# Kernel optimization log

Hardware: AMD Instinct MI355X
Metric: run time of the kernel (lower is better)

Reference implementation:

```python
import jax, jax.numpy as jnp
import numpy as np

DECAY = 0.99
EPS = 1e-05
THRESHOLD = 2.0
CODEBOOK_SIZE = 2048
DIM = 256


def setup_inputs() -> dict:
    key = jax.random.key(0)
    k1, k2, k3 = jax.random.split(key, 3)
    x = jax.random.normal(k1, (32, 1500, DIM), dtype=jnp.float32)
    # kaiming_uniform_ with a=0: bound = sqrt(6 / fan_in)
    bound = float(np.sqrt(6.0 / DIM))
    embed = jax.random.uniform(k2, (CODEBOOK_SIZE, DIM), dtype=jnp.float32,
                               minval=-bound, maxval=bound)
    # warm EMA state: positive cluster sizes, consistent embed_avg
    cluster_size = jax.random.uniform(k3, (CODEBOOK_SIZE,), dtype=jnp.float32,
                                      minval=0.0, maxval=200.0)
    embed_avg = embed * cluster_size[:, None]
    return {"x": x, "embed": embed, "cluster_size": cluster_size,
            "embed_avg": embed_avg}


def reference(x, embed, cluster_size, embed_avg):
    shape = x.shape
    K = embed.shape[0]
    xf = x.reshape(-1, shape[-1])                       # [N, D]

    # quantize: negative squared Euclidean distance, argmax == argmin dist
    x2 = jnp.sum(xf * xf, axis=1, keepdims=True)        # [N, 1]
    e2 = jnp.sum(embed * embed, axis=1)                 # [K]
    dist = -(x2 - 2.0 * (xf @ embed.T) + e2[None, :])   # [N, K]
    embed_ind = jnp.argmax(dist, axis=-1)               # [N]

    # dequantize (embedding gather)
    quantize = embed[embed_ind].reshape(shape)          # [B, T, D]

    # training-path EMA statistics (onehot.sum(0) and x.T @ onehot, as segment sums)
    counts = jax.ops.segment_sum(jnp.ones(xf.shape[0], dtype=x.dtype),
                                 embed_ind, num_segments=K)        # [K]
    embed_sum = jax.ops.segment_sum(xf, embed_ind, num_segments=K) # [K, D]

    new_cluster_size = cluster_size * DECAY + (1.0 - DECAY) * counts
    new_embed_avg = embed_avg * DECAY + (1.0 - DECAY) * embed_sum

    n = new_cluster_size.sum()
    smoothed = (new_cluster_size + EPS) / (n + K * EPS) * n
    embed_normalized = new_embed_avg / smoothed[:, None]

    # dead-code expiration: replace expired codes with random batch vectors
    expired = new_cluster_size < THRESHOLD
    perm = jax.random.permutation(jax.random.key(1), xf.shape[0])[:K]
    replacement = xf[perm]                              # [K, D]
    new_embed = jnp.where(expired[:, None], replacement, embed_normalized)

    codes = embed_ind.reshape(shape[:-1])               # [B, T]
    return quantize, codes, new_cluster_size, new_embed_avg, new_embed
```

## Files before the change

kernel.cpp:

```cpp
#include <hip/hip_runtime.h>
#include <hip/hip_bf16.h>
#include <stdint.h>
#include <math.h>

#define N_TOK 48000
#define DIMS  256
#define KCB   2048
#define WND 0.10f
#define BIAS 32.0f

typedef __attribute__((ext_vector_type(8))) short bf16x8;
typedef __attribute__((ext_vector_type(4))) float f32x4;
typedef __attribute__((ext_vector_type(8))) unsigned short u16x8;

__device__ __forceinline__ unsigned short bf16rn(float f) {
  uint32_t u = __float_as_uint(f);
  uint32_t r = (u + 0x7FFFu + ((u >> 16) & 1u)) >> 16;
  return (unsigned short)r;
}

__device__ __forceinline__ uint32_t packBiased(float fb, uint32_t invIdx) {
  float c = fmaxf(fb, 0.0f);
  return (__float_as_uint(c) & ~0x7FFu) | invIdx;
}
__device__ __forceinline__ uint32_t packThrBiased(float fb) {
  float c = fmaxf(fb, 0.0f);
  return __float_as_uint(c) & ~0x7FFu;
}
__device__ __forceinline__ float unpackBiased(uint32_t u) {
  return __uint_as_float(u & ~0x7FFu);
}
__device__ __forceinline__ void ins3u(uint32_t& b, uint32_t& s, uint32_t& t, uint32_t v) {
  uint32_t lo = min(b, v);
  b = max(b, v);
  uint32_t lo2 = min(s, lo);
  s = max(s, lo);
  t = max(t, lo2);
}

__device__ inline void tf2x32(uint32_t k0, uint32_t k1, uint32_t c0, uint32_t c1,
                              uint32_t& o0, uint32_t& o1) {
  uint32_t ks2 = k0 ^ k1 ^ 0x1BD11BDAu;
  uint32_t x0 = c0 + k0, x1 = c1 + k1;
#define TF_R(r) { x0 += x1; x1 = (x1 << (r)) | (x1 >> (32 - (r))); x1 ^= x0; }
  TF_R(13) TF_R(15) TF_R(26) TF_R(6)
  x0 += k1; x1 += ks2 + 1u;
  TF_R(17) TF_R(29) TF_R(16) TF_R(24)
  x0 += ks2; x1 += k0 + 2u;
  TF_R(13) TF_R(15) TF_R(26) TF_R(6)
  x0 += k0; x1 += k1 + 3u;
  TF_R(17) TF_R(29) TF_R(16) TF_R(24)
  x0 += k1; x1 += ks2 + 4u;
  TF_R(13) TF_R(15) TF_R(26) TF_R(6)
  x0 += ks2; x1 += k0 + 5u;
#undef TF_R
  o0 = x0; o1 = x1;
}

__device__ inline void get_round_key(int round, uint32_t& ka, uint32_t& kb) {
  const uint32_t b0 = 0u, b1 = 1u;
  uint32_t K1a, K1b, S1a, S1b;
  tf2x32(b0, b1, 0u, 0u, K1a, K1b);
  tf2x32(b0, b1, 0u, 1u, S1a, S1b);
  if (round == 1) { ka = S1a; kb = S1b; return; }
  uint32_t S2a, S2b;
  tf2x32(K1a, K1b, 0u, 1u, S2a, S2b);
  ka = S2a; kb = S2b;
}

__device__ inline uint32_t gen_key(int round, uint32_t i) {
  uint32_t ka, kb, o0, o1;
  get_round_key(round, ka, kb);
  tf2x32(ka, kb, 0u, i, o0, o1);
  return o0 ^ o1;
}

__device__ __forceinline__ void gload_lds16(const void* g, void* l) {
  __builtin_amdgcn_global_load_lds(
      (const __attribute__((address_space(1))) uint32_t*)g,
      (__attribute__((address_space(3))) uint32_t*)l, 16, 0, 0);
}

__global__ void e2split_keys(const float* __restrict__ x, unsigned short* __restrict__ xh,
                             const float* __restrict__ embed, unsigned short* __restrict__ eh,
                             float* __restrict__ e2f, double* __restrict__ e2d,
                             uint32_t* __restrict__ keys1, uint32_t* __restrict__ keys2,
                             uint32_t* __restrict__ bcount1, uint32_t* __restrict__ bcount2) {
  const int nx = N_TOK * DIMS / 8;
  const int ne = KCB * DIMS / 8;
  int i = blockIdx.x * blockDim.x + threadIdx.x;
  if (i < nx + ne) {
    const float* src; unsigned short* dst; int j;
    if (i < nx) { src = x; dst = xh; j = i; }
    else { src = embed; dst = eh; j = i - nx; }
    float4 a = ((const float4*)src)[j * 2];
    float4 b = ((const float4*)src)[j * 2 + 1];
    float v[8] = {a.x, a.y, a.z, a.w, b.x, b.y, b.z, b.w};
    u16x8 h;
#pragma unroll
    for (int q = 0; q < 8; ++q) h[q] = bf16rn(v[q]);
    *(u16x8*)&dst[(size_t)j * 8] = h;
    return;
  }
  int k = i - (nx + ne);
  if (k < KCB) {
    const float4* er = (const float4*)(embed + (size_t)k * DIMS);
    float s = 0.f;
    double sd = 0.0;
    for (int c = 0; c < DIMS / 4; ++c) {
      float4 v = er[c];
      s = fmaf(v.x, v.x, s); s = fmaf(v.y, v.y, s);
      s = fmaf(v.z, v.z, s); s = fmaf(v.w, v.w, s);
      sd += (double)v.x * v.x + (double)v.y * v.y
          + (double)v.z * v.z + (double)v.w * v.w;
    }
    e2f[k] = BIAS - s;
    e2d[k] = sd;
    return;
  }
  int n = k - KCB;
  if (n < N_TOK) {
    uint32_t k1 = gen_key(1, (uint32_t)n);
    uint32_t k2 = gen_key(2, (uint32_t)n);
    keys1[n] = k1; keys2[n] = k2;
    atomicAdd(&bcount1[k1 >> 21], 1u);
    atomicAdd(&bcount2[k2 >> 21], 1u);
  }
}

__global__ __launch_bounds__(256, 2) void dist_mfma(
    const unsigned short* __restrict__ xh, const unsigned short* __restrict__ eh,
    const float* __restrict__ e2f,
    uint32_t* __restrict__ pb, uint32_t* __restrict__ ps, uint32_t* __restrict__ pt)
{
  __shared__ __align__(16) char smem[50688];
  short (*As)[128 * 32] = (short(*)[128 * 32])smem;
  short (*Bs)[256 * 32] = (short(*)[256 * 32])(smem + 16384);
  uint32_t* red = (uint32_t*)smem;

  const int tid = threadIdx.x;
  const int lane = tid & 63, w = tid >> 6;
  const int wr = w >> 1, wc = w & 1;
  const int l15 = lane & 15, lg = lane >> 4;

  int bx, by;
  {
    const int bid = blockIdx.x;
    if (bid < 2944) { int g = bid >> 6, r = bid & 63; bx = g * 8 + (r & 7); by = r >> 3; }
    else            { int t2 = bid - 2944; bx = 368 + (t2 % 7); by = t2 / 7; }
  }
  const int n0 = bx * 128;
  const int c0 = by * 256;

  f32x4 acc[4][8];
#pragma unroll
  for (int mf = 0; mf < 4; ++mf)
#pragma unroll
    for (int nf = 0; nf < 8; ++nf) acc[mf][nf] = (f32x4){0.f, 0.f, 0.f, 0.f};

  auto stage = [&](int t) {
    const int d0 = t << 5;
    const int q = t & 1;
#pragma unroll
    for (int i = 0; i < 2; ++i) {
      const int c = i * 256 + tid;
      const int row = c >> 2;
      const int sc = ((c & 3) ^ ((row >> 1) & 3)) << 3;
      gload_lds16(xh + (size_t)(n0 + row) * DIMS + d0 + sc, (void*)&As[q][c * 8]);
    }
#pragma unroll
    for (int i = 0; i < 4; ++i) {
      const int c = i * 256 + tid;
      const int row = c >> 2;
      const int sc = ((c & 3) ^ ((row >> 1) & 3)) << 3;
      gload_lds16(eh + (size_t)(c0 + row) * DIMS + d0 + sc, (void*)&Bs[q][c * 8]);
    }
  };

  stage(0);
  __syncthreads();

#pragma unroll 1
  for (int t = 0; t < 8; ++t) {
    if (t < 7) stage(t + 1);
    const int q = t & 1;
    bf16x8 af[4], bfv[8];
#pragma unroll
    for (int mf = 0; mf < 4; ++mf) {
      const int r = wr * 64 + mf * 16 + l15;
      af[mf] = *(const bf16x8*)&As[q][r * 32 + ((lg ^ ((r >> 1) & 3)) << 3)];
    }
#pragma unroll
    for (int nf = 0; nf < 8; ++nf) {
      const int r = wc * 128 + nf * 16 + l15;
      bfv[nf] = *(const bf16x8*)&Bs[q][r * 32 + ((lg ^ ((r >> 1) & 3)) << 3)];
    }
#pragma unroll
    for (int mf = 0; mf < 4; ++mf)
#pragma unroll
      for (int nf = 0; nf < 8; ++nf)
        acc[mf][nf] = __builtin_amdgcn_mfma_f32_16x16x32_bf16(
            af[mf], bfv[nf], acc[mf][nf], 0, 0, 0);
    __syncthreads();
  }

  float e2v[8];
  uint32_t inv[8];
#pragma unroll
  for (int nf = 0; nf < 8; ++nf) {
    int k = c0 + wc * 128 + nf * 16 + l15;
    e2v[nf] = e2f[k];
    inv[nf] = 2047u - (uint32_t)k;
  }

  const int colbase = wc * 16 + l15;
#pragma unroll
  for (int mf = 0; mf < 4; ++mf) {
#pragma unroll
    for (int reg = 0; reg < 4; ++reg) {
      uint32_t p0 = packBiased(fmaf(2.f, acc[mf][0][reg], e2v[0]), inv[0]);
      uint32_t p1 = packBiased(fmaf(2.f, acc[mf][1][reg], e2v[1]), inv[1]);
      uint32_t p2 = packBiased(fmaf(2.f, acc[mf][2][reg], e2v[2]), inv[2]);
      uint32_t h1 = max(p0, p1), l1 = min(p0, p1);
      uint32_t b  = max(h1, p2), m  = min(h1, p2);
      uint32_t s  = max(l1, m),  t3 = min(l1, m);
#pragma unroll
      for (int nf = 3; nf < 8; ++nf) {
        float f = fmaf(2.f, acc[mf][nf][reg], e2v[nf]);
        ins3u(b, s, t3, packBiased(f, inv[nf]));
      }
      const int row = wr * 64 + mf * 16 + lg * 4 + reg;
      uint32_t* p = &red[row * 99 + colbase * 3];
      p[0] = b; p[1] = s; p[2] = t3;
    }
  }
  __syncthreads();
  {
    const int row = tid >> 1, half = tid & 1;
    uint32_t b = 0u, s = 0u, t3 = 0u;
    const uint32_t* p = &red[row * 99 + half * 48];
#pragma unroll 4
    for (int c = 0; c < 48; ++c) ins3u(b, s, t3, p[c]);
    if (half) {
      uint32_t* q = &red[row * 99 + 96];
      q[0] = b; q[1] = s; q[2] = t3;
    }
    __syncthreads();
    if (!half) {
      const uint32_t* q = &red[row * 99 + 96];
      ins3u(b, s, t3, q[0]);
      ins3u(b, s, t3, q[1]);
      ins3u(b, s, t3, q[2]);
      size_t o = (size_t)by * N_TOK + n0 + row;
      pb[o] = b; ps[o] = s; pt[o] = t3;
    }
  }
}

__global__ void merge8(const uint32_t* __restrict__ pb, const uint32_t* __restrict__ ps,
                       const uint32_t* __restrict__ pt,
                       int* __restrict__ ind,
                       int* __restrict__ candRows, int* __restrict__ candIdx,
                       int* __restrict__ candCnt, int* __restrict__ listC,
                       uint32_t* __restrict__ cntA, uint32_t* __restrict__ cntC) {
  int n = blockIdx.x * blockDim.x + threadIdx.x;
  if (n >= N_TOK) return;
  uint32_t tb[8], tsv[8], ttv[8];
#pragma unroll
  for (int tt = 0; tt < 8; ++tt) {
    size_t o = (size_t)tt * N_TOK + n;
    tb[tt] = pb[o]; tsv[tt] = ps[o]; ttv[tt] = pt[o];
  }
  uint32_t best = tb[0];
#pragma unroll
  for (int tt = 1; tt < 8; ++tt) best = max(best, tb[tt]);
  ind[n] = 2047 - (int)(best & 0x7FFu);
  const uint32_t thr = packThrBiased(unpackBiased(best) - WND);
  int m = 0; bool full = false;
#pragma unroll
  for (int tt = 0; tt < 8; ++tt) {
    m += (tb[tt] >= thr) + (tsv[tt] >= thr);
    full = full || (ttv[tt] >= thr);
  }
  if (full) {
    listC[atomicAdd(cntC, 1u)] = n;
  } else if (m > 1) {
    uint32_t i = atomicAdd(cntA, 1u);
    candRows[i] = n; candCnt[i] = m;
    int j = 0;
#pragma unroll
    for (int tt = 0; tt < 8; ++tt) {
      if (tb[tt]  >= thr) candIdx[(size_t)i * 16 + (j++)] = 2047 - (int)(tb[tt]  & 0x7FFu);
      if (tsv[tt] >= thr) candIdx[(size_t)i * 16 + (j++)] = 2047 - (int)(tsv[tt] & 0x7FFu);
    }
  }
}

#define RC_BLOCKS 512
#define RF_BLOCKS 1024
__global__ void refine_both(const float* __restrict__ x, const float* __restrict__ embed,
                            const double* __restrict__ e2d,
                            const int* __restrict__ candRows, const int* __restrict__ candIdx,
                            const int* __restrict__ candCnt,
                            const int* __restrict__ listC,
                            const uint32_t* __restrict__ cntAB,
                            int* __restrict__ ind) {
  __shared__ double xd[DIMS];
  __shared__ double rv[256];
  __shared__ int    rk[256];
  const int tid = threadIdx.x;
  if (blockIdx.x < RC_BLOCKS) {
    const uint32_t nA = cntAB[0];
    const int lane = tid & 63;
    const uint32_t wid = ((uint32_t)blockIdx.x * 256 + tid) >> 6;
    const uint32_t nw = RC_BLOCKS * 4;
    for (uint32_t i = wid; i < nA; i += nw) {
      const int n = candRows[i];
      const int m = candCnt[i];
      float4 xv = ((const float4*)x)[(size_t)n * 64 + lane];
      double best = -1e300; int bk = 0x7fffffff;
      for (int j = 0; j < m; ++j) {
        int k = candIdx[(size_t)i * 16 + j];
        float4 e4 = ((const float4*)embed)[(size_t)k * 64 + lane];
        double d = (double)xv.x * e4.x + (double)xv.y * e4.y
                 + (double)xv.z * e4.z + (double)xv.w * e4.w;
#pragma unroll
        for (int mm = 1; mm < 64; mm <<= 1) d += __shfl_xor(d, mm);
        double v = 2.0 * d - e2d[k];
        if (v > best || (v == best && k < bk)) { best = v; bk = k; }
      }
      if (lane == 0) ind[n] = bk;
    }
    return;
  }
  const uint32_t nC = cntAB[1];
  for (uint32_t it = blockIdx.x - RC_BLOCKS; it < nC; it += RF_BLOCKS) {
    const int n = listC[it];
    __syncthreads();
    xd[tid] = (double)x[(size_t)n * DIMS + tid];
    __syncthreads();
    double best = -1e300; int bk = 0x7fffffff;
    for (int k = tid; k < KCB; k += 256) {
      const float4* er = (const float4*)(embed + (size_t)k * DIMS);
      double a0 = 0.0, a1 = 0.0, a2 = 0.0, a3 = 0.0;
      for (int c = 0; c < 64; c += 4) {
        float4 ea = er[c], eb = er[c + 1], ec = er[c + 2], ed = er[c + 3];
        int d = c * 4;
        a0 += xd[d + 0] * ea.x + xd[d + 1] * ea.y + xd[d + 2] * ea.z + xd[d + 3] * ea.w;
        a1 += xd[d + 4] * eb.x + xd[d + 5] * eb.y + xd[d + 6] * eb.z + xd[d + 7] * eb.w;
        a2 += xd[d + 8] * ec.x + xd[d + 9] * ec.y + xd[d + 10] * ec.z + xd[d + 11] * ec.w;
        a3 += xd[d + 12] * ed.x + xd[d + 13] * ed.y + xd[d + 14] * ed.z + xd[d + 15] * ed.w;
      }
      double v = 2.0 * (a0 + a1 + a2 + a3) - e2d[k];
      if (v > best || (v == best && k < bk)) { best = v; bk = k; }
    }
    rv[tid] = best; rk[tid] = bk;
    __syncthreads();
    for (int s = 128; s > 0; s >>= 1) {
      if (tid < s) {
        double v2 = rv[tid + s]; int k2 = rk[tid + s];
        if (v2 > rv[tid] || (v2 == rv[tid] && k2 < rk[tid])) { rv[tid] = v2; rk[tid] = k2; }
      }
      __syncthreads();
    }
    if (tid == 0) ind[n] = rk[0];
  }
}

__global__ void gather_q(const float* __restrict__ embed, const int* __restrict__ ind,
                         float* __restrict__ outq, float* __restrict__ outcodes,
                         uint32_t* __restrict__ cntTok) {
  int idx = blockIdx.x * blockDim.x + threadIdx.x;
  if (idx >= N_TOK * 64) return;
  int n = idx >> 6, c = idx & 63;
  int k = ind[n];
  ((float4*)outq)[idx] = ((const float4*)embed)[(size_t)k * 64 + c];
  if (c == 0) { outcodes[n] = (float)k; atomicAdd(&cntTok[k], 1u); }
}

__global__ void scan3(const uint32_t* __restrict__ cntTok, uint32_t* __restrict__ tokBase,
                      uint32_t* __restrict__ tokCur,
                      const float* __restrict__ cs, float* __restrict__ out_ncs,
                      int* __restrict__ expired, double* __restrict__ nsum,
                      const uint32_t* __restrict__ bcount1, uint32_t* __restrict__ bbase1,
                      uint32_t* __restrict__ cursor1,
                      const uint32_t* __restrict__ bcount2, uint32_t* __restrict__ bbase2,
                      uint32_t* __restrict__ cursor2) {
  __shared__ uint32_t buf[2][2048];
  __shared__ double sd[1024];
  int t = threadIdx.x;
  const uint32_t* in; uint32_t* out; uint32_t* cz;
  if (blockIdx.x == 0)      { in = cntTok;  out = tokBase; cz = tokCur;  }
  else if (blockIdx.x == 1) { in = bcount1; out = bbase1;  cz = cursor1; }
  else                      { in = bcount2; out = bbase2;  cz = cursor2; }
  double local = 0.0;
  for (int q = 0; q < 2; ++q) {
    int i = t + q * 1024;
    uint32_t c = in[i];
    buf[0][i] = c;
    cz[i] = 0;
    if (blockIdx.x == 0) {
      double v = 0.99 * (double)cs[i] + 0.01 * (double)c;
      out_ncs[i] = (float)v;
      expired[i] = (v < 2.0) ? 1 : 0;
      local += v;
    }
  }
  if (blockIdx.x == 0) sd[t] = local;
  __syncthreads();
  int src = 0;
  for (int off = 1; off < 2048; off <<= 1) {
    for (int q = 0; q < 2; ++q) {
      int i = t + q * 1024;
      uint32_t v = buf[src][i];
      if (i >= off) v += buf[src][i - off];
      buf[src ^ 1][i] = v;
    }
    src ^= 1; __syncthreads();
  }
  for (int q = 0; q < 2; ++q) {
    int i = t + q * 1024;
    out[i] = buf[src][i] - in[i];
  }
  if (blockIdx.x == 0) {
    for (int s = 512; s > 0; s >>= 1) { if (t < s) sd[t] += sd[t + s]; __syncthreads(); }
    if (t == 0) nsum[0] = sd[0];
  }
}

__global__ void scatter_both(const int* __restrict__ ind, const uint32_t* __restrict__ tokBase,
                             uint32_t* __restrict__ tokCur, uint32_t* __restrict__ tokBucket,
                             const uint32_t* __restrict__ keys1, const uint32_t* __restrict__ bbase1,
                             uint32_t* __restrict__ cursor1,
                             uint32_t* __restrict__ bkey, uint32_t* __restrict__ bval) {
  int n = blockIdx.x * blockDim.x + threadIdx.x;
  if (n >= N_TOK) return;
  int k = ind[n];
  uint32_t p = atomicAdd(&tokCur[k], 1u);
  tokBucket[tokBase[k] + p] = (uint32_t)n;
  uint32_t k1 = keys1[n];
  uint32_t b = k1 >> 21;
  uint32_t q = atomicAdd(&cursor1[b], 1u);
  uint32_t s = bbase1[b] + q;
  bkey[s] = k1; bval[s] = (uint32_t)n;
}

#define ES_BLOCKS 512
__global__ void esum_rank1(const float* __restrict__ x, const uint32_t* __restrict__ tokBase,
                           const uint32_t* __restrict__ cntTok,
                           const uint32_t* __restrict__ tokBucket,
                           float* __restrict__ esum,
                           const uint32_t* __restrict__ bkey, const uint32_t* __restrict__ bval,
                           const uint32_t* __restrict__ bbase1, const uint32_t* __restrict__ bcount1,
                           const uint32_t* __restrict__ keys2,
                           const uint32_t* __restrict__ bbase2, uint32_t* __restrict__ cursor2,
                           uint32_t* __restrict__ bkey2, uint32_t* __restrict__ bval2,
                           uint32_t* __restrict__ bpos2) {
  const int tid = threadIdx.x;
  if (blockIdx.x < ES_BLOCKS) {
    const uint32_t wv = ((uint32_t)blockIdx.x * 256 + tid) >> 6;
    const int lane = tid & 63;
    const uint32_t base = tokBase[wv], cnt = cntTok[wv];
    float4 a0 = {0.f, 0.f, 0.f, 0.f}, a1 = {0.f, 0.f, 0.f, 0.f};
    uint32_t i = 0;
    for (; i + 2 <= cnt; i += 2) {
      uint32_t n0 = tokBucket[base + i], n1 = tokBucket[base + i + 1];
      float4 v0 = ((const float4*)x)[(size_t)n0 * 64 + lane];
      float4 v1 = ((const float4*)x)[(size_t)n1 * 64 + lane];
      a0.x += v0.x; a0.y += v0.y; a0.z += v0.z; a0.w += v0.w;
      a1.x += v1.x; a1.y += v1.y; a1.z += v1.z; a1.w += v1.w;
    }
    if (i < cnt) {
      uint32_t n0 = tokBucket[base + i];
      float4 v0 = ((const float4*)x)[(size_t)n0 * 64 + lane];
      a0.x += v0.x; a0.y += v0.y; a0.z += v0.z; a0.w += v0.w;
    }
    float4 r; r.x = a0.x + a1.x; r.y = a0.y + a1.y; r.z = a0.z + a1.z; r.w = a0.w + a1.w;
    ((float4*)esum)[(size_t)wv * 64 + lane] = r;
    return;
  }
  int b = blockIdx.x - ES_BLOCKS;
  uint32_t base = bbase1[b], cnt = bcount1[b];
  for (uint32_t t = tid; t < cnt; t += 256) {
    uint32_t k = bkey[base + t], pv = bval[base + t];
    uint32_t r = 0;
    for (uint32_t j = 0; j < cnt; ++j) {
      uint32_t kj = bkey[base + j], pj = bval[base + j];
      r += (kj < k) | ((kj == k) & (pj < pv));
    }
    uint32_t p = base + r;
    uint32_t k2 = keys2[p];
    uint32_t b2 = k2 >> 21;
    uint32_t q = atomicAdd(&cursor2[b2], 1u);
    uint32_t s = bbase2[b2] + q;
    bkey2[s] = k2; bval2[s] = pv; bpos2[s] = p;
  }
}

__global__ void rank2(const uint32_t* __restrict__ bkey2, const uint32_t* __restrict__ bval2,
                      const uint32_t* __restrict__ bpos2,
                      const uint32_t* __restrict__ bbase2, const uint32_t* __restrict__ bcount2,
                      uint32_t* __restrict__ perm) {
  int b = blockIdx.x;
  uint32_t base = bbase2[b];
  if (base >= KCB) return;
  uint32_t cnt = bcount2[b];
  for (uint32_t t = threadIdx.x; t < cnt; t += blockDim.x) {
    uint32_t k = bkey2[base + t], p = bpos2[base + t];
    uint32_t r = 0;
    for (uint32_t j = 0; j < cnt; ++j) {
      uint32_t kj = bkey2[base + j], pj = bpos2[base + j];
      r += (kj < k) | ((kj == k) & (pj < p));
    }
    uint32_t pos = base + r;
    if (pos < KCB) perm[pos] = bval2[base + t];
  }
}

__global__ void final_embed(const float* __restrict__ x, const float* __restrict__ cs,
                            const uint32_t* __restrict__ cntTok,
                            const float* __restrict__ eavg, const float* __restrict__ esum,
                            const int* __restrict__ expired, const double* __restrict__ nsum,
                            const uint32_t* __restrict__ perm,
                            float* __restrict__ out_eavg, float* __restrict__ out_ne) {
  int idx = blockIdx.x * blockDim.x + threadIdx.x;
  if (idx >= KCB * 64) return;
  int k = idx >> 6, c = idx & 63;
  float4 ea = ((const float4*)eavg)[idx];
  float4 es = ((const float4*)esum)[idx];
  double ax = 0.99 * (double)ea.x + 0.01 * (double)es.x;
  double ay = 0.99 * (double)ea.y + 0.01 * (double)es.y;
  double az = 0.99 * (double)ea.z + 0.01 * (double)es.z;
  double aw = 0.99 * (double)ea.w + 0.01 * (double)es.w;
  float4 nv; nv.x = (float)ax; nv.y = (float)ay; nv.z = (float)az; nv.w = (float)aw;
  ((float4*)out_eavg)[idx] = nv;
  float4 r;
  if (expired[k]) {
    r = ((const float4*)x)[(size_t)perm[k] * 64 + c];
  } else {
    double ncs = 0.99 * (double)cs[k] + 0.01 * (double)cntTok[k];
    double n = nsum[0];
    double sm = (ncs + 1e-5) / (n + 2048.0 * 1e-5) * n;
    r.x = (float)(ax / sm); r.y = (float)(ay / sm);
    r.z = (float)(az / sm); r.w = (float)(aw / sm);
  }
  ((float4*)out_ne)[idx] = r;
}

extern "C" void kernel_launch(void* const* d_in, const int* in_sizes, int n_in,
                              void* d_out, int out_size, void* d_ws, size_t ws_size,
                              hipStream_t stream) {
  const float* x     = (const float*)d_in[0];
  const float* embed = (const float*)d_in[1];
  const float* cs    = (const float*)d_in[2];
  const float* eavg  = (const float*)d_in[3];

  float* out = (float*)d_out;
  float* outQ    = out;
  float* outC    = out + 12288000;
  float* outNCS  = out + 12336000;
  float* outEAVG = out + 12338048;
  float* outNE   = out + 12862336;

  char* w = (char*)d_ws;
  size_t off = 0;
  auto alloc = [&](size_t bytes) -> void* {
    void* p = w + off; off += (bytes + 255) & ~(size_t)255; return p;
  };
  unsigned short* xh = (unsigned short*)alloc((size_t)N_TOK * DIMS * 2);
  unsigned short* eh = (unsigned short*)alloc((size_t)KCB * DIMS * 2);
  float*    e2f     = (float*)alloc(KCB * 4);
  double*   e2d     = (double*)alloc(KCB * 8);
  float*    esum    = (float*)alloc((size_t)KCB * DIMS * 4);
  uint32_t* pbest   = (uint32_t*)alloc((size_t)8 * N_TOK * 4);
  uint32_t* psecond = (uint32_t*)alloc((size_t)8 * N_TOK * 4);
  uint32_t* pthird  = (uint32_t*)alloc((size_t)8 * N_TOK * 4);
  int*      ind     = (int*)alloc(N_TOK * 4);
  int*      candRows= (int*)alloc(N_TOK * 4);
  int*      candCnt = (int*)alloc(N_TOK * 4);
  int*      candIdx = (int*)alloc((size_t)N_TOK * 16 * 4);
  int*      listC   = (int*)alloc(N_TOK * 4);
  double*   nsum    = (double*)alloc(256);
  int*      expired = (int*)alloc(KCB * 4);
  uint32_t* tokBase = (uint32_t*)alloc(KCB * 4);
  uint32_t* tokCur  = (uint32_t*)alloc(KCB * 4);
  uint32_t* tokBucket = (uint32_t*)alloc(N_TOK * 4);
  uint32_t* keys1   = (uint32_t*)alloc(N_TOK * 4);
  uint32_t* keys2   = (uint32_t*)alloc(N_TOK * 4);
  uint32_t* bkey    = (uint32_t*)alloc(N_TOK * 4);
  uint32_t* bval    = (uint32_t*)alloc(N_TOK * 4);
  uint32_t* bkey2   = (uint32_t*)alloc(N_TOK * 4);
  uint32_t* bval2   = (uint32_t*)alloc(N_TOK * 4);
  uint32_t* bpos2   = (uint32_t*)alloc(N_TOK * 4);
  uint32_t* bbase1  = (uint32_t*)alloc(KCB * 4);
  uint32_t* bbase2  = (uint32_t*)alloc(KCB * 4);
  uint32_t* cursor1 = (uint32_t*)alloc(KCB * 4);
  uint32_t* cursor2 = (uint32_t*)alloc(KCB * 4);
  uint32_t* perm    = (uint32_t*)alloc(KCB * 4);
  uint32_t* cntAB   = (uint32_t*)alloc(256);
  uint32_t* cntTok  = (uint32_t*)alloc(KCB * 4);
  uint32_t* bcount1 = (uint32_t*)alloc(KCB * 4);
  uint32_t* bcount2 = (uint32_t*)alloc(KCB * 4);

  hipMemsetAsync(cntAB, 0, 256 + 3 * KCB * 4, stream);

  e2split_keys<<<(N_TOK * DIMS / 8 + KCB * DIMS / 8 + KCB + N_TOK + 255) / 256, 256, 0,
                 stream>>>(x, xh, embed, eh, e2f, e2d, keys1, keys2, bcount1, bcount2);

  dist_mfma<<<3000, 256, 0, stream>>>(xh, eh, e2f, pbest, psecond, pthird);
  merge8<<<188, 256, 0, stream>>>(pbest, psecond, pthird,
                                  ind, candRows, candIdx, candCnt, listC,
                                  &cntAB[0], &cntAB[1]);
  refine_both<<<RC_BLOCKS + RF_BLOCKS, 256, 0, stream>>>(
      x, embed, e2d, candRows, candIdx, candCnt, listC, cntAB, ind);

  gather_q<<<12000, 256, 0, stream>>>(embed, ind, outQ, outC, cntTok);
  scan3<<<3, 1024, 0, stream>>>(cntTok, tokBase, tokCur, cs, outNCS, expired, nsum,
                                bcount1, bbase1, cursor1, bcount2, bbase2, cursor2);
  scatter_both<<<188, 256, 0, stream>>>(ind, tokBase, tokCur, tokBucket,
                                        keys1, bbase1, cursor1, bkey, bval);
  esum_rank1<<<ES_BLOCKS + KCB, 256, 0, stream>>>(
      x, tokBase, cntTok, tokBucket, esum,
      bkey, bval, bbase1, bcount1, keys2, bbase2, cursor2, bkey2, bval2, bpos2);
  rank2<<<2048, 64, 0, stream>>>(bkey2, bval2, bpos2, bbase2, bcount2, perm);

  final_embed<<<512, 256, 0, stream>>>(x, cs, cntTok, eavg, esum, expired, nsum,
                                       perm, outEAVG, outNE);
}
```

Baseline: 235.5 us.

## Fuse gather into scan kernel, move code counting upstream, use med3 top-3 insert

The top-3 insertion in the distance kernel now uses v_max3/v_med3/v_min3 instructions, which cuts the VALU op count per candidate. Writing the codes and the per-code token count moves out of the gather kernel and into merge8 (for tokens not needing refinement) and refine_both (for refined tokens). The embedding gather is then merged into the scan kernel as extra blocks, removing one launch and letting the gather run alongside the three scan blocks. The cost is 1024-thread blocks for the gather and a split atomic-count path that must count every token exactly once.

```diff
diff --git a/kernel.cpp b/kernel.cpp
--- a/kernel.cpp
+++ b/kernel.cpp
@@ -19,6 +19,19 @@
   return (unsigned short)r;
 }
 
+__device__ __forceinline__ uint32_t max3u(uint32_t a, uint32_t b, uint32_t c) {
+  uint32_t d; asm("v_max3_u32 %0, %1, %2, %3" : "=v"(d) : "v"(a), "v"(b), "v"(c));
+  return d;
+}
+__device__ __forceinline__ uint32_t med3u(uint32_t a, uint32_t b, uint32_t c) {
+  uint32_t d; asm("v_med3_u32 %0, %1, %2, %3" : "=v"(d) : "v"(a), "v"(b), "v"(c));
+  return d;
+}
+__device__ __forceinline__ uint32_t min3u(uint32_t a, uint32_t b, uint32_t c) {
+  uint32_t d; asm("v_min3_u32 %0, %1, %2, %3" : "=v"(d) : "v"(a), "v"(b), "v"(c));
+  return d;
+}
+
 __device__ __forceinline__ uint32_t packBiased(float fb, uint32_t invIdx) {
   float c = fmaxf(fb, 0.0f);
   return (__float_as_uint(c) & ~0x7FFu) | invIdx;
@@ -31,11 +44,10 @@
   return __uint_as_float(u & ~0x7FFu);
 }
 __device__ __forceinline__ void ins3u(uint32_t& b, uint32_t& s, uint32_t& t, uint32_t v) {
-  uint32_t lo = min(b, v);
+  uint32_t b0 = b;
   b = max(b, v);
-  uint32_t lo2 = min(s, lo);
-  s = max(s, lo);
-  t = max(t, lo2);
+  t = max(t, min3u(b0, s, v));
+  s = med3u(b0, s, v);
 }
 
 __device__ inline void tf2x32(uint32_t k0, uint32_t k1, uint32_t c0, uint32_t c1,
@@ -221,9 +233,9 @@
       uint32_t p0 = packBiased(fmaf(2.f, acc[mf][0][reg], e2v[0]), inv[0]);
       uint32_t p1 = packBiased(fmaf(2.f, acc[mf][1][reg], e2v[1]), inv[1]);
       uint32_t p2 = packBiased(fmaf(2.f, acc[mf][2][reg], e2v[2]), inv[2]);
-      uint32_t h1 = max(p0, p1), l1 = min(p0, p1);
-      uint32_t b  = max(h1, p2), m  = min(h1, p2);
-      uint32_t s  = max(l1, m),  t3 = min(l1, m);
+      uint32_t b  = max3u(p0, p1, p2);
+      uint32_t s  = med3u(p0, p1, p2);
+      uint32_t t3 = min3u(p0, p1, p2);
 #pragma unroll
       for (int nf = 3; nf < 8; ++nf) {
         float f = fmaf(2.f, acc[mf][nf][reg], e2v[nf]);
@@ -262,7 +274,8 @@
                        int* __restrict__ ind,
                        int* __restrict__ candRows, int* __restrict__ candIdx,
                        int* __restrict__ candCnt, int* __restrict__ listC,
-                       uint32_t* __restrict__ cntA, uint32_t* __restrict__ cntC) {
+                       uint32_t* __restrict__ cntA, uint32_t* __restrict__ cntC,
+                       float* __restrict__ outcodes, uint32_t* __restrict__ cntTok) {
   int n = blockIdx.x * blockDim.x + threadIdx.x;
   if (n >= N_TOK) return;
   uint32_t tb[8], tsv[8], ttv[8];
@@ -274,7 +287,8 @@
   uint32_t best = tb[0];
 #pragma unroll
   for (int tt = 1; tt < 8; ++tt) best = max(best, tb[tt]);
-  ind[n] = 2047 - (int)(best & 0x7FFu);
+  int kb = 2047 - (int)(best & 0x7FFu);
+  ind[n] = kb;
   const uint32_t thr = packThrBiased(unpackBiased(best) - WND);
   int m = 0; bool full = false;
 #pragma unroll
@@ -293,6 +307,9 @@
       if (tb[tt]  >= thr) candIdx[(size_t)i * 16 + (j++)] = 2047 - (int)(tb[tt]  & 0x7FFu);
       if (tsv[tt] >= thr) candIdx[(size_t)i * 16 + (j++)] = 2047 - (int)(tsv[tt] & 0x7FFu);
     }
+  } else {
+    outcodes[n] = (float)kb;
+    atomicAdd(&cntTok[kb], 1u);
   }
 }
 
@@ -304,7 +321,8 @@
                             const int* __restrict__ candCnt,
                             const int* __restrict__ listC,
                             const uint32_t* __restrict__ cntAB,
-                            int* __restrict__ ind) {
+                            int* __restrict__ ind,
+                            float* __restrict__ outcodes, uint32_t* __restrict__ cntTok) {
   __shared__ double xd[DIMS];
   __shared__ double rv[256];
   __shared__ int    rk[256];
@@ -329,7 +347,11 @@
         double v = 2.0 * d - e2d[k];
         if (v > best || (v == best && k < bk)) { best = v; bk = k; }
       }
-      if (lane == 0) ind[n] = bk;
+      if (lane == 0) {
+        ind[n] = bk;
+        outcodes[n] = (float)bk;
+        atomicAdd(&cntTok[bk], 1u);
+      }
     }
     return;
   }
@@ -363,32 +385,35 @@
       }
       __syncthreads();
     }
-    if (tid == 0) ind[n] = rk[0];
-  }
-}
-
-__global__ void gather_q(const float* __restrict__ embed, const int* __restrict__ ind,
-                         float* __restrict__ outq, float* __restrict__ outcodes,
-                         uint32_t* __restrict__ cntTok) {
-  int idx = blockIdx.x * blockDim.x + threadIdx.x;
-  if (idx >= N_TOK * 64) return;
-  int n = idx >> 6, c = idx & 63;
-  int k = ind[n];
-  ((float4*)outq)[idx] = ((const float4*)embed)[(size_t)k * 64 + c];
-  if (c == 0) { outcodes[n] = (float)k; atomicAdd(&cntTok[k], 1u); }
-}
-
-__global__ void scan3(const uint32_t* __restrict__ cntTok, uint32_t* __restrict__ tokBase,
-                      uint32_t* __restrict__ tokCur,
-                      const float* __restrict__ cs, float* __restrict__ out_ncs,
-                      int* __restrict__ expired, double* __restrict__ nsum,
-                      const uint32_t* __restrict__ bcount1, uint32_t* __restrict__ bbase1,
-                      uint32_t* __restrict__ cursor1,
-                      const uint32_t* __restrict__ bcount2, uint32_t* __restrict__ bbase2,
-                      uint32_t* __restrict__ cursor2) {
+    if (tid == 0) {
+      ind[n] = rk[0];
+      outcodes[n] = (float)rk[0];
+      atomicAdd(&cntTok[rk[0]], 1u);
+    }
+  }
+}
+
+__global__ void gather_scan(const float* __restrict__ embed, const int* __restrict__ ind,
+                            float* __restrict__ outq,
+                            const uint32_t* __restrict__ cntTok, uint32_t* __restrict__ tokBase,
+                            uint32_t* __restrict__ tokCur,
+                            const float* __restrict__ cs, float* __restrict__ out_ncs,
+                            int* __restrict__ expired, double* __restrict__ nsum,
+                            const uint32_t* __restrict__ bcount1, uint32_t* __restrict__ bbase1,
+                            uint32_t* __restrict__ cursor1,
+                            const uint32_t* __restrict__ bcount2, uint32_t* __restrict__ bbase2,
+                            uint32_t* __restrict__ cursor2) {
   __shared__ uint32_t buf[2][2048];
   __shared__ double sd[1024];
-  int t = threadIdx.x;
+  const int t = threadIdx.x;
+  if (blockIdx.x >= 3) {
+    int idx = (blockIdx.x - 3) * 1024 + t;
+    if (idx < N_TOK * 64) {
+      int n = idx >> 6, c = idx & 63;
+      ((float4*)outq)[idx] = ((const float4*)embed)[(size_t)ind[n] * 64 + c];
+    }
+    return;
+  }
   const uint32_t* in; uint32_t* out; uint32_t* cz;
   if (blockIdx.x == 0)      { in = cntTok;  out = tokBase; cz = tokCur;  }
   else if (blockIdx.x == 1) { in = bcount1; out = bbase1;  cz = cursor1; }
@@ -610,13 +635,14 @@
   dist_mfma<<<3000, 256, 0, stream>>>(xh, eh, e2f, pbest, psecond, pthird);
   merge8<<<188, 256, 0, stream>>>(pbest, psecond, pthird,
                                   ind, candRows, candIdx, candCnt, listC,
-                                  &cntAB[0], &cntAB[1]);
+                                  &cntAB[0], &cntAB[1], outC, cntTok);
   refine_both<<<RC_BLOCKS + RF_BLOCKS, 256, 0, stream>>>(
-      x, embed, e2d, candRows, candIdx, candCnt, listC, cntAB, ind);
-
-  gather_q<<<12000, 256, 0, stream>>>(embed, ind, outQ, outC, cntTok);
-  scan3<<<3, 1024, 0, stream>>>(cntTok, tokBase, tokCur, cs, outNCS, expired, nsum,
-                                bcount1, bbase1, cursor1, bcount2, bbase2, cursor2);
+      x, embed, e2d, candRows, candIdx, candCnt, listC, cntAB, ind, outC, cntTok);
+
+  gather_scan<<<3 + (N_TOK * 64 + 1023) / 1024, 1024, 0, stream>>>(
+      embed, ind, outQ,
+      cntTok, tokBase, tokCur, cs, outNCS, expired, nsum,
+      bcount1, bbase1, cursor1, bcount2, bbase2, cursor2);
   scatter_both<<<188, 256, 0, stream>>>(ind, tokBase, tokCur, tokBucket,
                                         keys1, bbase1, cursor1, bkey, bval);
   esum_rank1<<<ES_BLOCKS + KCB, 256, 0, stream>>>(
```

Measured after the change: 226.3 us. 3.9% less time.
